# Kernel optimization log

Measured on AMD Instinct MI355X. Metric: run time of the kernel, lower is better.

The kernel has to match this reference:

```python
import jax, jax.numpy as jnp
import numpy as np

NH = 8      # num_heads
DK = 160    # total key/query depth
DV = 64     # total value depth
DKH = DK // NH  # 20
DVH = DV // NH  # 8


def conv2d(x, w, b, pad):
    y = jax.lax.conv_general_dilated(
        x, w, window_strides=(1, 1), padding=[(pad, pad), (pad, pad)],
        dimension_numbers=('NCHW', 'OIHW', 'NCHW'))
    return y + b[None, :, None, None]


def rel_to_abs(x):
    # x: (B, Hd, L, 2L-1) -> (B, Hd, L, L)
    B, Hd, L, _ = x.shape
    x = jnp.pad(x, ((0, 0), (0, 0), (0, 0), (0, 1)))          # (B,Hd,L,2L)
    flat = x.reshape(B, Hd, L * 2 * L)
    flat = jnp.pad(flat, ((0, 0), (0, 0), (0, L - 1)))
    final = flat.reshape(B, Hd, L + 1, 2 * L - 1)
    return final[:, :, :L, L - 1:]


def relative_logits_1d(q, rel_k, H, W, perm):
    # q: (B, NH, H, W, DKH); NOTE: einsum output drops head axis -> sums over heads,
    # exactly as in the torch source ('bhxyd,md->bxym').
    rl = jnp.einsum('bhxyd,md->bxym', q, rel_k)               # (B,H,W,2W-1)
    rl = rel_to_abs(rl.reshape(-1, H, W, 2 * W - 1))          # (B,H,W,W)
    B = rl.shape[0]
    rl = rl[:, None, :, None, :, :]                           # (B,1,H,1,W,W)
    rl = jnp.broadcast_to(rl, (B, NH, H, H, W, W))
    rl = jnp.transpose(rl, perm)
    return rl.reshape(B, NH, H * W, H * W)


def setup_inputs() -> dict:
    key = jax.random.key(0)
    ks = jax.random.split(key, 9)
    s = 0.05
    return {
        'x': jax.random.normal(ks[0], (8, 256, 32, 32), jnp.float32),
        'kqv_w': jax.random.normal(ks[1], (384, 256, 1, 1), jnp.float32) * s,
        'kqv_b': jax.random.normal(ks[2], (384,), jnp.float32) * s,
        'conv_out_w': jax.random.normal(ks[3], (192, 256, 3, 3), jnp.float32) * s,
        'conv_out_b': jax.random.normal(ks[4], (192,), jnp.float32) * s,
        'attn_w': jax.random.normal(ks[5], (64, 64, 1, 1), jnp.float32) * s,
        'attn_b': jax.random.normal(ks[6], (64,), jnp.float32) * s,
        'rel_h': jax.random.normal(ks[7], (63, 20), jnp.float32),
        'rel_w': jax.random.normal(ks[8], (63, 20), jnp.float32),
    }


def reference(x, kqv_w, kqv_b, conv_out_w, conv_out_b, attn_w, attn_b, rel_h, rel_w):
    B, C, H, W = x.shape
    kqv = conv2d(x, kqv_w, kqv_b, 0)
    k, q, v = kqv[:, :DK], kqv[:, DK:2 * DK], kqv[:, 2 * DK:]
    q = q * (DKH ** -0.5)
    # split_heads_2d in the source is a raw reshape (no transpose); replicate exactly
    k = k.reshape(B, NH, H, W, DKH)
    q = q.reshape(B, NH, H, W, DKH)
    v = v.reshape(B, NH, H, W, DVH)
    qf = q.reshape(B, NH, H * W, DKH)
    kf = k.reshape(B, NH, H * W, DKH)
    vf = v.reshape(B, NH, H * W, DVH)
    qk = jnp.einsum('bnid,bnjd->bnij', qf, kf)                # (B,NH,HW,HW)
    qr_w_l = relative_logits_1d(q, rel_w, H, W, (0, 1, 2, 4, 3, 5))
    qr_h_l = relative_logits_1d(jnp.swapaxes(q, 2, 3), rel_h, W, H, (0, 1, 4, 2, 5, 3))
    weights = jax.nn.softmax(qk + qr_h_l + qr_w_l, axis=-1)
    attn = jnp.matmul(weights, vf)                            # (B,NH,HW,DVH)
    attn = attn.reshape(B, NH, DVH, H, W).reshape(B, DV, H, W)  # raw reshapes as in source
    attn = conv2d(attn, attn_w, attn_b, 0)
    return jnp.concatenate([conv2d(x, conv_out_w, conv_out_b, 1), attn], axis=1)
```

## Files before the change

kernel.cpp:

```cpp
#include <hip/hip_runtime.h>

constexpr float QSCALE = 0.22360679774997896f;
constexpr float LOG2E  = 1.4426950408889634f;

typedef __attribute__((ext_vector_type(8))) short bf16x8;
typedef __attribute__((ext_vector_type(4))) float f32x4;

__device__ __forceinline__ unsigned short f2bf(float f) {
    unsigned u = __float_as_uint(f);
    u = (u + 0x7FFFu + ((u >> 16) & 1u)) >> 16;
    return (unsigned short)u;
}

__device__ __forceinline__ unsigned cvt_pk_bf16(float lo, float hi) {
    unsigned r;
    asm("v_cvt_pk_bf16_f32 %0, %1, %2" : "=v"(r) : "v"(lo), "v"(hi));
    return r;
}

__device__ __forceinline__ void qk_decomp(unsigned flat, int& n, int& i, int& d) {
    n = flat / 20480u;
    unsigned r = flat - (unsigned)n * 20480u;
    i = r / 20u;
    d = r - (unsigned)i * 20u;
}

__global__ __launch_bounds__(256) void pack_inputs_kernel(
    const float* __restrict__ X, const float* __restrict__ Wconv,
    const float* __restrict__ Wkqv, unsigned short* __restrict__ Xt2,
    unsigned short* __restrict__ Xq, unsigned short* __restrict__ Wp,
    unsigned short* __restrict__ Wq, unsigned short* __restrict__ Kb,
    unsigned short* __restrict__ Qb, unsigned short* __restrict__ VtF)
{
    int t = blockIdx.x * 256 + threadIdx.x;
    if (t < 295936) {
        int b = t / 36992, rem = t - b * 36992;
        int chunk = rem / 4624; int rem2 = rem - chunk * 4624;
        int kc = rem2 / 1156;   int spad = rem2 - kc * 1156;
        int yp = spad / 34, xp = spad - yp * 34;
        bf16x8 v = {};
        if (yp >= 1 && yp <= 32 && xp >= 1 && xp <= 32) {
            const float* src = X + (size_t)b * 262144
                                 + (size_t)(chunk * 32 + kc * 8) * 1024
                                 + (yp - 1) * 32 + (xp - 1);
            #pragma unroll
            for (int j = 0; j < 8; ++j) v[j] = (short)f2bf(src[(size_t)j * 1024]);
        }
        *(bf16x8*)&Xt2[(((size_t)b * 8 + chunk) * 1156 + spad) * 32 + kc * 8] = v;
    } else if (t < 558080) {
        int t2 = t - 295936;
        int lane = t2 & 63;
        int chunk = (t2 >> 6) & 7;
        int g16 = (t2 >> 9) & 63;
        int b = t2 >> 15;
        int sp = g16 * 16 + (lane & 15);
        const float* src = X + (size_t)b * 262144
                             + (size_t)(chunk * 32 + (lane >> 4) * 8) * 1024 + sp;
        bf16x8 v;
        #pragma unroll
        for (int j = 0; j < 8; ++j) v[j] = (short)f2bf(src[(size_t)j * 1024]);
        *(bf16x8*)&Xq[(size_t)t2 * 8] = v;
    } else if (t < 613376) {
        int t2 = t - 558080;
        int l = t2 & 63;
        int rb = (t2 >> 6) & 3;
        int ks = (t2 >> 8) % 72;
        int ot = t2 / 18432;
        int oc = ot * 64 + rb * 16 + (l & 15);
        int kbase = ks * 32 + (l >> 4) * 8;
        bf16x8 v;
        #pragma unroll
        for (int j = 0; j < 8; ++j) {
            int kp = kbase + j;
            int r = kp >> 8, c = kp & 255;
            v[j] = (short)f2bf(Wconv[((size_t)oc * 256 + c) * 9 + r]);
        }
        *(bf16x8*)&Wp[(size_t)t2 * 8] = v;
    } else if (t < 625664) {
        int t2 = t - 613376;
        int l = t2 & 63;
        int rb = (t2 >> 6) & 3;
        int ks = (t2 >> 8) & 7;
        int ot = t2 / 2048;
        int oc = ot * 64 + rb * 16 + (l & 15);
        float sc = (oc >= 160 && oc < 320) ? QSCALE : 1.0f;
        int kbase = ks * 32 + (l >> 4) * 8;
        bf16x8 v;
        #pragma unroll
        for (int j = 0; j < 8; ++j)
            v[j] = (short)f2bf(Wkqv[(size_t)oc * 256 + kbase + j] * sc);
        *(bf16x8*)&Wq[(size_t)t2 * 8] = v;
    } else if (t < 691200) {
        int row = t - 625664;
        bf16x8 z = {};
        *(uint2*)&Kb[(size_t)row * 32 + 20] = make_uint2(0u, 0u);
        *(bf16x8*)&Kb[(size_t)row * 32 + 24] = z;
    } else if (t < 756736) {
        int row = t - 691200;
        bf16x8 z = {};
        *(uint2*)&Qb[(size_t)row * 32 + 20] = make_uint2(0u, 0u);
        *(bf16x8*)&Qb[(size_t)row * 32 + 24] = z;
    } else {
        int t2 = t - 756736;
        int bn = t2 >> 10;
        int G = (t2 >> 5) & 31;
        int r8 = (t2 >> 2) & 7;
        int ksub = t2 & 3;
        unsigned short fill = (r8 == 0) ? 0x3F80 : 0;
        bf16x8 v = {short(fill), short(fill), short(fill), short(fill),
                    short(fill), short(fill), short(fill), short(fill)};
        *(bf16x8*)&VtF[(((size_t)bn * 32 + G) * 64 + (8 + r8) + ksub * 16) * 8] = v;
    }
}

__global__ __launch_bounds__(256) void mfma_gemms_kernel(
    const unsigned short* __restrict__ Wp, const unsigned short* __restrict__ Wq,
    const unsigned short* __restrict__ Xt2, const unsigned short* __restrict__ Xq,
    const float* __restrict__ cbias, const float* __restrict__ qbias,
    float* __restrict__ out, float* __restrict__ qf32,
    unsigned short* __restrict__ Kb, unsigned short* __restrict__ Qb,
    unsigned short* __restrict__ VtF)
{
    const int b  = blockIdx.z;
    const int ty = blockIdx.y;
    const int s0 = blockIdx.x * 64;
    const int tid = threadIdx.x;
    const int lane = tid & 63, w = tid >> 6;
    const int wr = w >> 1, wc = w & 1;
    const int kc = lane >> 4, ln = lane & 15;

    f32x4 acc00 = {}, acc01 = {}, acc10 = {}, acc11 = {};
    const int scol = s0 + wc * 32 + ln;

    if (ty < 3) {
        const int Y = blockIdx.x * 2;
        const size_t aoff0 = ((size_t)(ty * 288 + wr * 2) * 64 + lane) * 8;
        const size_t aoff1 = aoff0 + 512;
        const int spad0 = (Y + wc + 1) * 34 + 1 + ln;
        const unsigned short* xb = Xt2 + (size_t)b * 8 * 36992;

        #pragma unroll 1
        for (int cc = 0; cc < 8; ++cc) {
            bf16x8 A0[9], A1[9];
            #pragma unroll
            for (int r = 0; r < 9; ++r) {
                A0[r] = *(const bf16x8*)&Wp[aoff0 + (size_t)(r * 8 + cc) * 2048];
                A1[r] = *(const bf16x8*)&Wp[aoff1 + (size_t)(r * 8 + cc) * 2048];
            }
            const unsigned short* xc = xb + (size_t)cc * 36992 + kc * 8;
            #pragma unroll
            for (int r = 0; r < 9; ++r) {
                const int off = (r / 3 - 1) * 34 + (r % 3 - 1);
                const unsigned short* bp = xc + (size_t)(spad0 + off) * 32;
                bf16x8 b0 = *(const bf16x8*)bp;
                bf16x8 b1 = *(const bf16x8*)(bp + 512);
                acc00 = __builtin_amdgcn_mfma_f32_16x16x32_bf16(A0[r], b0, acc00, 0, 0, 0);
                acc01 = __builtin_amdgcn_mfma_f32_16x16x32_bf16(A0[r], b1, acc01, 0, 0, 0);
                acc10 = __builtin_amdgcn_mfma_f32_16x16x32_bf16(A1[r], b0, acc10, 0, 0, 0);
                acc11 = __builtin_amdgcn_mfma_f32_16x16x32_bf16(A1[r], b1, acc11, 0, 0, 0);
            }
        }

        const int ocb = ty * 64 + wr * 32;
        float* ob = out + (size_t)b * 262144;
        #pragma unroll
        for (int r = 0; r < 4; ++r) {
            int oc0 = ocb + kc * 4 + r;
            float b0v = cbias[oc0];
            ob[(size_t)oc0 * 1024 + scol]      = acc00[r] + b0v;
            ob[(size_t)oc0 * 1024 + scol + 16] = acc01[r] + b0v;
            int oc1 = oc0 + 16;
            float b1v = cbias[oc1];
            ob[(size_t)oc1 * 1024 + scol]      = acc10[r] + b1v;
            ob[(size_t)oc1 * 1024 + scol + 16] = acc11[r] + b1v;
        }
    } else {
        const int ot = ty - 3;
        const size_t aoff0 = ((size_t)(ot * 32 + wr * 2) * 64 + lane) * 8;
        const size_t aoff1 = aoff0 + 512;
        const int g0 = blockIdx.x * 4 + wc * 2;
        const size_t xb0 = (((size_t)b * 64 + g0) * 8) * 512 + lane * 8;
        const size_t xb1 = xb0 + 4096;

        #pragma unroll
        for (int cc = 0; cc < 8; ++cc) {
            bf16x8 a0 = *(const bf16x8*)&Wq[aoff0 + (size_t)cc * 2048];
            bf16x8 a1 = *(const bf16x8*)&Wq[aoff1 + (size_t)cc * 2048];
            bf16x8 b0 = *(const bf16x8*)&Xq[xb0 + (size_t)cc * 512];
            bf16x8 b1 = *(const bf16x8*)&Xq[xb1 + (size_t)cc * 512];
            acc00 = __builtin_amdgcn_mfma_f32_16x16x32_bf16(a0, b0, acc00, 0, 0, 0);
            acc01 = __builtin_amdgcn_mfma_f32_16x16x32_bf16(a0, b1, acc01, 0, 0, 0);
            acc10 = __builtin_amdgcn_mfma_f32_16x16x32_bf16(a1, b0, acc10, 0, 0, 0);
            acc11 = __builtin_amdgcn_mfma_f32_16x16x32_bf16(a1, b1, acc11, 0, 0, 0);
        }

        const int ocb = ot * 64 + wr * 32;
        const int b8 = b * 8;
        #pragma unroll
        for (int r = 0; r < 4; ++r) {
            #pragma unroll
            for (int e = 0; e < 4; ++e) {
                int oc  = ocb + (e >> 1) * 16 + kc * 4 + r;
                int col = scol + (e & 1) * 16;
                float val = (e == 0) ? acc00[r] : (e == 1) ? acc01[r]
                          : (e == 2) ? acc10[r] : acc11[r];
                if (oc < 160) {
                    float v = val + qbias[oc];
                    int n, i, d; qk_decomp((unsigned)oc * 1024u + col, n, i, d);
                    Kb[(((size_t)(b8 + n) * 1024 + i) << 5) + d] = f2bf(v);
                } else if (oc < 320) {
                    float v = val + qbias[oc] * QSCALE;
                    unsigned flat = (unsigned)(oc - 160) * 1024u + col;
                    qf32[(size_t)b * 163840 + flat] = v;
                    int n, i, d; qk_decomp(flat, n, i, d);
                    Qb[(((size_t)(b8 + n) * 1024 + i) << 5) + d] = f2bf(v * LOG2E);
                } else {
                    float v = val + qbias[oc];
                    unsigned flat = (unsigned)(oc - 320) * 1024u + col;
                    int n = flat >> 13, i = (flat >> 3) & 1023, dd = flat & 7;
                    int G = i >> 5, k0 = i & 31;
                    VtF[((((size_t)(b8 + n) * 32 + G) * 64) + dd + ((k0 >> 3) << 4)) * 8
                        + (k0 & 7)] = f2bf(v);
                }
            }
        }
    }
}

__global__ __launch_bounds__(256) void rel_kernel(
    const float* __restrict__ qf32,
    const float* __restrict__ rel_h, const float* __restrict__ rel_w,
    float* __restrict__ Rh, float* __restrict__ Rw)
{
    const int blk = blockIdx.x;
    const int b = blk >> 6, st = blk & 63;
    const int s0 = st * 16;
    const int tid = threadIdx.x;
    __shared__ float rhS[63][21];
    __shared__ float rwS[63][21];
    __shared__ float qs[16][20];

    for (int i = tid; i < 1260; i += 256) {
        int mm = i / 20, d = i - mm * 20;
        rhS[mm][d] = rel_h[i];
        rwS[mm][d] = rel_w[i];
    }
    for (int e = tid; e < 320; e += 256) {
        int s = e / 20, d = e - s * 20;
        const float* qb = qf32 + (size_t)b * 163840 + (s0 + s) * 20 + d;
        float acc = 0.0f;
        #pragma unroll
        for (int n = 0; n < 8; ++n) acc += qb[(size_t)n * 20480];
        qs[s][d] = acc;
    }
    __syncthreads();

    for (int p = tid; p < 1008; p += 256) {
        int s = p / 63, mm = p - s * 63;
        float sh = 0.0f, sw = 0.0f;
        #pragma unroll
        for (int d = 0; d < 20; ++d) {
            float qv = qs[s][d];
            sh += qv * rhS[mm][d];
            sw += qv * rwS[mm][d];
        }
        int sg = s0 + s;
        int y = sg >> 5, x = sg & 31;
        Rw[(size_t)b * 64512 + sg * 63 + mm] = sw * LOG2E;
        Rh[(size_t)b * 64512 + (x * 32 + y) * 63 + mm] = sh * LOG2E;
    }
}

__global__ __launch_bounds__(256, 4) void attn_mfma_kernel(
    const unsigned short* __restrict__ Qb, const unsigned short* __restrict__ Kb,
    const unsigned short* __restrict__ VtF, const float* __restrict__ Rh,
    const float* __restrict__ Rw, float* __restrict__ attnout)
{
    const int bn = blockIdx.y;
    const int b = bn >> 3;
    const int i0 = blockIdx.x * 64;
    const int tid = threadIdx.x;
    const int lane = tid & 63, w = tid >> 6;

    __shared__ float RhS[64][33];
    __shared__ float RwS[64][33];
    __shared__ unsigned short Pl[4][16][72];
    {
        int q = tid & 63, seg = tid >> 6;
        int i = i0 + q, y1 = i >> 5, x1 = i & 31;
        const float* rh = Rh + (size_t)b * 64512 + (x1 * 32 + y1) * 63 + 31 - y1 + seg * 8;
        const float* rw = Rw + (size_t)b * 64512 + i * 63 + 31 - x1 + seg * 8;
        #pragma unroll
        for (int j = 0; j < 8; ++j) {
            RhS[q][seg * 8 + j] = rh[j];
            RwS[q][seg * 8 + j] = rw[j];
        }
    }
    __syncthreads();

    const int ql = lane & 15, g = lane >> 4;
    const int qw = i0 + w * 16;

    bf16x8 qf = *(const bf16x8*)&Qb[((size_t)bn * 1024 + qw + ql) * 32 + g * 8];
    const unsigned short* kp = Kb + ((size_t)bn * 1024 + ql) * 32 + g * 8;
    const unsigned short* vp = VtF + (size_t)bn * 32 * 512 + lane * 8;

    const float* rhrow = &RhS[w * 16 + ql][0];
    float rwA[4], rwB[4];
    #pragma unroll
    for (int r = 0; r < 4; ++r) {
        rwA[r] = RwS[w * 16 + ql][4 * g + r];
        rwB[r] = RwS[w * 16 + ql][16 + 4 * g + r];
    }

    f32x4 oaccT = {};

    bf16x8 c0 = *(const bf16x8*)&kp[0 * 512];
    bf16x8 c1 = *(const bf16x8*)&kp[1 * 512];
    bf16x8 c2 = *(const bf16x8*)&kp[2 * 512];
    bf16x8 c3 = *(const bf16x8*)&kp[3 * 512];

    #pragma unroll 2
    for (int kt = 0; kt < 16; ++kt) {
        __builtin_amdgcn_s_setprio(1);
        f32x4 s0 = {}, s1 = {}, s2 = {}, s3 = {};
        s0 = __builtin_amdgcn_mfma_f32_16x16x32_bf16(c0, qf, s0, 0, 0, 0);
        s1 = __builtin_amdgcn_mfma_f32_16x16x32_bf16(c1, qf, s1, 0, 0, 0);
        s2 = __builtin_amdgcn_mfma_f32_16x16x32_bf16(c2, qf, s2, 0, 0, 0);
        s3 = __builtin_amdgcn_mfma_f32_16x16x32_bf16(c3, qf, s3, 0, 0, 0);
        __builtin_amdgcn_s_setprio(0);

        if (kt < 15) {
            kp += 2048;
            c0 = *(const bf16x8*)&kp[0 * 512];
            c1 = *(const bf16x8*)&kp[1 * 512];
            c2 = *(const bf16x8*)&kp[2 * 512];
            c3 = *(const bf16x8*)&kp[3 * 512];
        }

        float rh0 = rhrow[2 * kt];
        float rh1 = rhrow[2 * kt + 1];

        float p00 = exp2f(s0[0] + rh0 + rwA[0]), p01 = exp2f(s0[1] + rh0 + rwA[1]);
        float p02 = exp2f(s0[2] + rh0 + rwA[2]), p03 = exp2f(s0[3] + rh0 + rwA[3]);
        float p10 = exp2f(s1[0] + rh0 + rwB[0]), p11 = exp2f(s1[1] + rh0 + rwB[1]);
        float p12 = exp2f(s1[2] + rh0 + rwB[2]), p13 = exp2f(s1[3] + rh0 + rwB[3]);
        float p20 = exp2f(s2[0] + rh1 + rwA[0]), p21 = exp2f(s2[1] + rh1 + rwA[1]);
        float p22 = exp2f(s2[2] + rh1 + rwA[2]), p23 = exp2f(s2[3] + rh1 + rwA[3]);
        float p30 = exp2f(s3[0] + rh1 + rwB[0]), p31 = exp2f(s3[1] + rh1 + rwB[1]);
        float p32 = exp2f(s3[2] + rh1 + rwB[2]), p33 = exp2f(s3[3] + rh1 + rwB[3]);

        const int key = 4 * g;
        *(unsigned*)&Pl[w][ql][key]      = cvt_pk_bf16(p00, p01);
        *(unsigned*)&Pl[w][ql][key + 2]  = cvt_pk_bf16(p02, p03);
        *(unsigned*)&Pl[w][ql][key + 16] = cvt_pk_bf16(p10, p11);
        *(unsigned*)&Pl[w][ql][key + 18] = cvt_pk_bf16(p12, p13);
        *(unsigned*)&Pl[w][ql][key + 32] = cvt_pk_bf16(p20, p21);
        *(unsigned*)&Pl[w][ql][key + 34] = cvt_pk_bf16(p22, p23);
        *(unsigned*)&Pl[w][ql][key + 48] = cvt_pk_bf16(p30, p31);
        *(unsigned*)&Pl[w][ql][key + 50] = cvt_pk_bf16(p32, p33);

        #pragma unroll
        for (int half = 0; half < 2; ++half) {
            bf16x8 vfr = *(const bf16x8*)&vp[(size_t)(kt * 2 + half) * 512];
            bf16x8 pfr = *(const bf16x8*)&Pl[w][ql][half * 32 + g * 8];
            __builtin_amdgcn_s_setprio(1);
            oaccT = __builtin_amdgcn_mfma_f32_16x16x32_bf16(vfr, pfr, oaccT, 0, 0, 0);
            __builtin_amdgcn_s_setprio(0);
        }
    }

    float lsum = __shfl(oaccT[0], 32 + ql, 64);
    float inv = 1.0f / lsum;
    if (g < 2) {
        float4 o = {oaccT[0] * inv, oaccT[1] * inv, oaccT[2] * inv, oaccT[3] * inv};
        *(float4*)&attnout[((size_t)bn * 1024 + qw + ql) * 8 + g * 4] = o;
    }
}

__global__ __launch_bounds__(256) void attn_out_conv_kernel(
    const float* __restrict__ attn, const float* __restrict__ W,
    const float* __restrict__ bias, float* __restrict__ out)
{
    const int idx = blockIdx.x * 256 + threadIdx.x;
    const int b = idx >> 16, oc = (idx >> 10) & 63, s = idx & 1023;
    const float* ab = attn + (size_t)b * 65536;
    float sum = bias[oc];
    #pragma unroll
    for (int c = 0; c < 64; ++c)
        sum += W[oc * 64 + c] * ab[(size_t)c * 1024 + s];
    out[(size_t)b * 262144 + (size_t)(192 + oc) * 1024 + s] = sum;
}

extern "C" void kernel_launch(void* const* d_in, const int* in_sizes, int n_in,
                              void* d_out, int out_size, void* d_ws, size_t ws_size,
                              hipStream_t stream)
{
    const float* x          = (const float*)d_in[0];
    const float* kqv_w      = (const float*)d_in[1];
    const float* kqv_b      = (const float*)d_in[2];
    const float* conv_out_w = (const float*)d_in[3];
    const float* conv_out_b = (const float*)d_in[4];
    const float* attn_w     = (const float*)d_in[5];
    const float* attn_b     = (const float*)d_in[6];
    const float* rel_h      = (const float*)d_in[7];
    const float* rel_w      = (const float*)d_in[8];
    float* out = (float*)d_out;
    float* ws  = (float*)d_ws;

    float* ws_qf32 = ws;
    float* ws_rw   = ws + 1310720;
    float* ws_rh   = ws + 1826816;
    float* ws_attn = ws + 2342912;
    unsigned short* Qb  = (unsigned short*)(ws + 2867200);
    unsigned short* Kb  = (unsigned short*)(ws + 3915776);
    unsigned short* VtF = (unsigned short*)(ws + 4964352);
    unsigned short* Xt2 = (unsigned short*)(ws + 5488640);
    unsigned short* Xq  = (unsigned short*)(ws + 6672384);
    unsigned short* Wp  = (unsigned short*)(ws + 7720960);
    unsigned short* Wq  = (unsigned short*)(ws + 7942144);

    pack_inputs_kernel<<<3212, 256, 0, stream>>>(
        x, conv_out_w, kqv_w, Xt2, Xq, Wp, Wq, Kb, Qb, VtF);
    mfma_gemms_kernel<<<dim3(16, 9, 8), 256, 0, stream>>>(
        Wp, Wq, Xt2, Xq, conv_out_b, kqv_b, out, ws_qf32, Kb, Qb, VtF);
    rel_kernel<<<512, 256, 0, stream>>>(ws_qf32, rel_h, rel_w, ws_rh, ws_rw);
    attn_mfma_kernel<<<dim3(16, 64), 256, 0, stream>>>(
        Qb, Kb, VtF, ws_rh, ws_rw, ws_attn);
    attn_out_conv_kernel<<<2048, 256, 0, stream>>>(ws_attn, attn_w, attn_b, out);
}
```

Before: 90.32 us.

## Split conv K-loop across 8 waves and use MFMA for attention output conv

The 3x3 conv GEMM block grows to 512 threads. Two wave groups each handle half of the input-channel chunks, and their partial accumulators are combined through shared memory. The kqv path is re-tiled so each wave covers one 16-column group. The scalar fp32 1x1 attention-output conv becomes a bf16 MFMA kernel, with its weights pre-packed in the input pack kernel. This targets the long serial K-loop in the conv and the FMA-bound output projection, at the cost of a shared-memory reduction with a barrier and bf16 rounding of the attention output.

```diff
diff --git a/kernel.cpp b/kernel.cpp
--- a/kernel.cpp
+++ b/kernel.cpp
@@ -27,10 +27,11 @@
 
 __global__ __launch_bounds__(256) void pack_inputs_kernel(
     const float* __restrict__ X, const float* __restrict__ Wconv,
-    const float* __restrict__ Wkqv, unsigned short* __restrict__ Xt2,
-    unsigned short* __restrict__ Xq, unsigned short* __restrict__ Wp,
-    unsigned short* __restrict__ Wq, unsigned short* __restrict__ Kb,
-    unsigned short* __restrict__ Qb, unsigned short* __restrict__ VtF)
+    const float* __restrict__ Wkqv, const float* __restrict__ Wattn,
+    unsigned short* __restrict__ Xt2, unsigned short* __restrict__ Xq,
+    unsigned short* __restrict__ Wp, unsigned short* __restrict__ Wq,
+    unsigned short* __restrict__ Kb, unsigned short* __restrict__ Qb,
+    unsigned short* __restrict__ VtF, unsigned short* __restrict__ Wa)
 {
     int t = blockIdx.x * 256 + threadIdx.x;
     if (t < 295936) {
@@ -100,7 +101,7 @@
         bf16x8 z = {};
         *(uint2*)&Qb[(size_t)row * 32 + 20] = make_uint2(0u, 0u);
         *(bf16x8*)&Qb[(size_t)row * 32 + 24] = z;
-    } else {
+    } else if (t < 822272) {
         int t2 = t - 756736;
         int bn = t2 >> 10;
         int G = (t2 >> 5) & 31;
@@ -110,10 +111,22 @@
         bf16x8 v = {short(fill), short(fill), short(fill), short(fill),
                     short(fill), short(fill), short(fill), short(fill)};
         *(bf16x8*)&VtF[(((size_t)bn * 32 + G) * 64 + (8 + r8) + ksub * 16) * 8] = v;
-    }
-}
-
-__global__ __launch_bounds__(256) void mfma_gemms_kernel(
+    } else {
+        int t2 = t - 822272;
+        int l = t2 & 63;
+        int rb = (t2 >> 6) & 3;
+        int kchunk = t2 >> 8;
+        int oc = rb * 16 + (l & 15);
+        int kbase = kchunk * 32 + (l >> 4) * 8;
+        bf16x8 v;
+        #pragma unroll
+        for (int j = 0; j < 8; ++j)
+            v[j] = (short)f2bf(Wattn[(size_t)oc * 64 + kbase + j]);
+        *(bf16x8*)&Wa[(size_t)t2 * 8] = v;
+    }
+}
+
+__global__ __launch_bounds__(512) void mfma_gemms_kernel(
     const unsigned short* __restrict__ Wp, const unsigned short* __restrict__ Wq,
     const unsigned short* __restrict__ Xt2, const unsigned short* __restrict__ Xq,
     const float* __restrict__ cbias, const float* __restrict__ qbias,
@@ -126,13 +139,15 @@
     const int s0 = blockIdx.x * 64;
     const int tid = threadIdx.x;
     const int lane = tid & 63, w = tid >> 6;
-    const int wr = w >> 1, wc = w & 1;
     const int kc = lane >> 4, ln = lane & 15;
 
+    __shared__ float comb[4][64][17];
+
     f32x4 acc00 = {}, acc01 = {}, acc10 = {}, acc11 = {};
-    const int scol = s0 + wc * 32 + ln;
 
     if (ty < 3) {
+        const int kh = w >> 2, wr = (w >> 1) & 1, wc = w & 1;
+        const int wq = wr * 2 + wc;
         const int Y = blockIdx.x * 2;
         const size_t aoff0 = ((size_t)(ty * 288 + wr * 2) * 64 + lane) * 8;
         const size_t aoff1 = aoff0 + 512;
@@ -140,7 +155,8 @@
         const unsigned short* xb = Xt2 + (size_t)b * 8 * 36992;
 
         #pragma unroll 1
-        for (int cc = 0; cc < 8; ++cc) {
+        for (int cc2 = 0; cc2 < 4; ++cc2) {
+            const int cc = kh * 4 + cc2;
             bf16x8 A0[9], A1[9];
             #pragma unroll
             for (int r = 0; r < 9; ++r) {
@@ -161,49 +177,68 @@
             }
         }
 
-        const int ocb = ty * 64 + wr * 32;
-        float* ob = out + (size_t)b * 262144;
-        #pragma unroll
-        for (int r = 0; r < 4; ++r) {
-            int oc0 = ocb + kc * 4 + r;
-            float b0v = cbias[oc0];
-            ob[(size_t)oc0 * 1024 + scol]      = acc00[r] + b0v;
-            ob[(size_t)oc0 * 1024 + scol + 16] = acc01[r] + b0v;
-            int oc1 = oc0 + 16;
-            float b1v = cbias[oc1];
-            ob[(size_t)oc1 * 1024 + scol]      = acc10[r] + b1v;
-            ob[(size_t)oc1 * 1024 + scol + 16] = acc11[r] + b1v;
+        if (kh == 1) {
+            float* c0 = &comb[wq][lane][0];
+            #pragma unroll
+            for (int r = 0; r < 4; ++r) {
+                c0[r]      = acc00[r];
+                c0[4 + r]  = acc01[r];
+                c0[8 + r]  = acc10[r];
+                c0[12 + r] = acc11[r];
+            }
+        }
+        __syncthreads();
+        if (kh == 0) {
+            const float* c0 = &comb[wq][lane][0];
+            #pragma unroll
+            for (int r = 0; r < 4; ++r) {
+                acc00[r] += c0[r];
+                acc01[r] += c0[4 + r];
+                acc10[r] += c0[8 + r];
+                acc11[r] += c0[12 + r];
+            }
+            const int ocb = ty * 64 + wr * 32;
+            const int scol = s0 + wc * 32 + ln;
+            float* ob = out + (size_t)b * 262144;
+            #pragma unroll
+            for (int r = 0; r < 4; ++r) {
+                int oc0 = ocb + kc * 4 + r;
+                float b0v = cbias[oc0];
+                ob[(size_t)oc0 * 1024 + scol]      = acc00[r] + b0v;
+                ob[(size_t)oc0 * 1024 + scol + 16] = acc01[r] + b0v;
+                int oc1 = oc0 + 16;
+                float b1v = cbias[oc1];
+                ob[(size_t)oc1 * 1024 + scol]      = acc10[r] + b1v;
+                ob[(size_t)oc1 * 1024 + scol + 16] = acc11[r] + b1v;
+            }
         }
     } else {
         const int ot = ty - 3;
+        const int wr = w >> 2, wc = w & 3;
         const size_t aoff0 = ((size_t)(ot * 32 + wr * 2) * 64 + lane) * 8;
         const size_t aoff1 = aoff0 + 512;
-        const int g0 = blockIdx.x * 4 + wc * 2;
+        const int g0 = blockIdx.x * 4 + wc;
         const size_t xb0 = (((size_t)b * 64 + g0) * 8) * 512 + lane * 8;
-        const size_t xb1 = xb0 + 4096;
 
         #pragma unroll
         for (int cc = 0; cc < 8; ++cc) {
             bf16x8 a0 = *(const bf16x8*)&Wq[aoff0 + (size_t)cc * 2048];
             bf16x8 a1 = *(const bf16x8*)&Wq[aoff1 + (size_t)cc * 2048];
             bf16x8 b0 = *(const bf16x8*)&Xq[xb0 + (size_t)cc * 512];
-            bf16x8 b1 = *(const bf16x8*)&Xq[xb1 + (size_t)cc * 512];
             acc00 = __builtin_amdgcn_mfma_f32_16x16x32_bf16(a0, b0, acc00, 0, 0, 0);
-            acc01 = __builtin_amdgcn_mfma_f32_16x16x32_bf16(a0, b1, acc01, 0, 0, 0);
             acc10 = __builtin_amdgcn_mfma_f32_16x16x32_bf16(a1, b0, acc10, 0, 0, 0);
-            acc11 = __builtin_amdgcn_mfma_f32_16x16x32_bf16(a1, b1, acc11, 0, 0, 0);
         }
 
         const int ocb = ot * 64 + wr * 32;
+        const int scol = s0 + wc * 16 + ln;
         const int b8 = b * 8;
         #pragma unroll
         for (int r = 0; r < 4; ++r) {
             #pragma unroll
-            for (int e = 0; e < 4; ++e) {
-                int oc  = ocb + (e >> 1) * 16 + kc * 4 + r;
-                int col = scol + (e & 1) * 16;
-                float val = (e == 0) ? acc00[r] : (e == 1) ? acc01[r]
-                          : (e == 2) ? acc10[r] : acc11[r];
+            for (int e = 0; e < 2; ++e) {
+                int oc  = ocb + e * 16 + kc * 4 + r;
+                float val = e ? acc10[r] : acc00[r];
+                int col = scol;
                 if (oc < 160) {
                     float v = val + qbias[oc];
                     int n, i, d; qk_decomp((unsigned)oc * 1024u + col, n, i, d);
@@ -378,18 +413,55 @@
     }
 }
 
-__global__ __launch_bounds__(256) void attn_out_conv_kernel(
-    const float* __restrict__ attn, const float* __restrict__ W,
+__global__ __launch_bounds__(256) void attn_out_mfma_kernel(
+    const unsigned short* __restrict__ Wa, const float* __restrict__ attn,
     const float* __restrict__ bias, float* __restrict__ out)
 {
-    const int idx = blockIdx.x * 256 + threadIdx.x;
-    const int b = idx >> 16, oc = (idx >> 10) & 63, s = idx & 1023;
-    const float* ab = attn + (size_t)b * 65536;
-    float sum = bias[oc];
+    const int b = blockIdx.y;
+    const int tid = threadIdx.x;
+    const int w = tid >> 6, lane = tid & 63;
+    const int sg = blockIdx.x * 4 + w;
+    const int kc = lane >> 4, ln = lane & 15;
+    const int s = sg * 16 + ln;
+
+    const float* ab = attn + (size_t)b * 65536 + s;
+
+    f32x4 acc0 = {}, acc1 = {}, acc2 = {}, acc3 = {};
     #pragma unroll
-    for (int c = 0; c < 64; ++c)
-        sum += W[oc * 64 + c] * ab[(size_t)c * 1024 + s];
-    out[(size_t)b * 262144 + (size_t)(192 + oc) * 1024 + s] = sum;
+    for (int kchunk = 0; kchunk < 2; ++kchunk) {
+        const int c0 = kchunk * 32 + kc * 8;
+        const float* cp = ab + (size_t)c0 * 1024;
+        bf16x8 bf;
+        #pragma unroll
+        for (int j = 0; j < 8; j += 2) {
+            unsigned u = cvt_pk_bf16(cp[(size_t)j * 1024], cp[(size_t)(j + 1) * 1024]);
+            bf[j]     = (short)u;
+            bf[j + 1] = (short)(u >> 16);
+        }
+
+        const unsigned short* wp = Wa + (size_t)kchunk * 2048;
+        bf16x8 a0 = *(const bf16x8*)&wp[(size_t)(0 * 64 + lane) * 8];
+        bf16x8 a1 = *(const bf16x8*)&wp[(size_t)(1 * 64 + lane) * 8];
+        bf16x8 a2 = *(const bf16x8*)&wp[(size_t)(2 * 64 + lane) * 8];
+        bf16x8 a3 = *(const bf16x8*)&wp[(size_t)(3 * 64 + lane) * 8];
+        acc0 = __builtin_amdgcn_mfma_f32_16x16x32_bf16(a0, bf, acc0, 0, 0, 0);
+        acc1 = __builtin_amdgcn_mfma_f32_16x16x32_bf16(a1, bf, acc1, 0, 0, 0);
+        acc2 = __builtin_amdgcn_mfma_f32_16x16x32_bf16(a2, bf, acc2, 0, 0, 0);
+        acc3 = __builtin_amdgcn_mfma_f32_16x16x32_bf16(a3, bf, acc3, 0, 0, 0);
+    }
+
+    float* ob = out + ((size_t)b * 256 + 192) * 1024 + s;
+    #pragma unroll
+    for (int r = 0; r < 4; ++r) {
+        int oc0 = 0 * 16 + kc * 4 + r;
+        int oc1 = 1 * 16 + kc * 4 + r;
+        int oc2 = 2 * 16 + kc * 4 + r;
+        int oc3 = 3 * 16 + kc * 4 + r;
+        ob[(size_t)oc0 * 1024] = acc0[r] + bias[oc0];
+        ob[(size_t)oc1 * 1024] = acc1[r] + bias[oc1];
+        ob[(size_t)oc2 * 1024] = acc2[r] + bias[oc2];
+        ob[(size_t)oc3 * 1024] = acc3[r] + bias[oc3];
+    }
 }
 
 extern "C" void kernel_launch(void* const* d_in, const int* in_sizes, int n_in,
@@ -419,13 +491,15 @@
     unsigned short* Xq  = (unsigned short*)(ws + 6672384);
     unsigned short* Wp  = (unsigned short*)(ws + 7720960);
     unsigned short* Wq  = (unsigned short*)(ws + 7942144);
-
-    pack_inputs_kernel<<<3212, 256, 0, stream>>>(
-        x, conv_out_w, kqv_w, Xt2, Xq, Wp, Wq, Kb, Qb, VtF);
-    mfma_gemms_kernel<<<dim3(16, 9, 8), 256, 0, stream>>>(
+    unsigned short* Wa  = (unsigned short*)(ws + 7991296);
+
+    pack_inputs_kernel<<<3214, 256, 0, stream>>>(
+        x, conv_out_w, kqv_w, attn_w, Xt2, Xq, Wp, Wq, Kb, Qb, VtF, Wa);
+    mfma_gemms_kernel<<<dim3(16, 9, 8), 512, 0, stream>>>(
         Wp, Wq, Xt2, Xq, conv_out_b, kqv_b, out, ws_qf32, Kb, Qb, VtF);
     rel_kernel<<<512, 256, 0, stream>>>(ws_qf32, rel_h, rel_w, ws_rh, ws_rw);
     attn_mfma_kernel<<<dim3(16, 64), 256, 0, stream>>>(
         Qb, Kb, VtF, ws_rh, ws_rw, ws_attn);
-    attn_out_conv_kernel<<<2048, 256, 0, stream>>>(ws_attn, attn_w, attn_b, out);
-}
+    attn_out_mfma_kernel<<<dim3(16, 8), 256, 0, stream>>>(
+        Wa, ws_attn, attn_b, out);
+}
```

Measured after the change: 94.88 us. 1.05x slower.
